# Performance work log

Hardware: AMD Instinct MI355X
Metric: run time of the kernel (lower is better)

The kernel has to match this reference:

```python
import jax, jax.numpy as jnp
import numpy as np

H_DIM = 32
EPS = 1e-7


def setup_inputs() -> dict:
    key = jax.random.key(0)
    ks = jax.random.split(key, 9)
    B, L, I = 2048, 256, 8
    return {
        "X": jax.random.normal(ks[0], (B, L, I), dtype=jnp.float32),
        "y": jax.random.randint(ks[1], (B,), 0, 2, dtype=jnp.int64),
        "W1": jax.random.normal(ks[2], (I, H_DIM), dtype=jnp.float32),
        "cls_tok": jax.random.normal(ks[3], (H_DIM,), dtype=jnp.float32),
        "W_q": jax.random.normal(ks[4], (H_DIM, H_DIM), dtype=jnp.float32),
        "W_k": jax.random.normal(ks[5], (H_DIM, H_DIM), dtype=jnp.float32),
        "W_v": jax.random.normal(ks[6], (H_DIM, H_DIM), dtype=jnp.float32),
        "W_t": jax.random.normal(ks[7], (H_DIM, H_DIM), dtype=jnp.float32),
        "W2": jax.random.normal(ks[8], (H_DIM, 2), dtype=jnp.float32),
    }


def reference(X, y, W1, cls_tok, W_q, W_k, W_v, W_t, W2):
    B = X.shape[0]
    # global mean/std normalization (torch.std is unbiased, ddof=1)
    h_pre1 = (X - X.mean()) / (X.std(ddof=1) + EPS)
    h_1 = h_pre1 @ W1                                   # [B, L, H]
    cls = jnp.broadcast_to(cls_tok[None, None, :], (B, 1, H_DIM))
    h_pre2 = jnp.concatenate([h_1, cls], axis=1)        # [B, L+1, H]
    Q = h_pre2 @ W_q
    K = h_pre2 @ W_k
    V = h_pre2 @ W_v
    S = jax.nn.softmax(jnp.einsum('bqh,bkh->bqk', Q, K) / jnp.sqrt(jnp.float32(H_DIM)), axis=-1)
    h_2 = jnp.einsum('bqk,bkh->bqh', S, V) + h_pre2 @ W_t
    z = h_2[:, -1] @ W2                                 # [B, o_dim]
    log_s = jax.nn.log_softmax(z, axis=-1)
    loss = -jnp.take_along_axis(log_s, y[:, None], axis=1)[:, 0].mean()
    return loss
```

## Files before the change

kernel.cpp:

```cpp
#include <hip/hip_runtime.h>

#define N_TOTAL 4194304
#define B_SIZE  2048
#define L_SIZE  256
#define I_DIM   8
#define H       32
#define K1_BLK  256

#define CRAW_OFF 4096
#define ACC_OFF  4112
#define FIXSCALE 4294967296.0
#define MASK56   0x00FFFFFFFFFFFFFFull

__global__ __launch_bounds__(1024) void k1_stats(
    const float4* __restrict__ X4,
    const float* __restrict__ W1, const float* __restrict__ cls,
    const float* __restrict__ Wq, const float* __restrict__ Wk,
    const float* __restrict__ Wv, const float* __restrict__ Wt,
    const float* __restrict__ W2, double* __restrict__ dws)
{
    const int t = threadIdx.x, b = blockIdx.x;
    const int lane = t & 63, wid = t >> 6;
    const int g = b * 1024 + t;

    float s1 = 0.f, s2 = 0.f;
    #pragma unroll
    for (int i = 0; i < 4; i++) {
        float4 v = X4[g + i * 262144];
        s1 += v.x + v.y + v.z + v.w;
        s2 += v.x * v.x + v.y * v.y + v.z * v.z + v.w * v.w;
    }
    for (int off = 32; off; off >>= 1) {
        s1 += __shfl_down(s1, off);
        s2 += __shfl_down(s2, off);
    }
    __shared__ float a1[16], a2[16];
    if (lane == 0) { a1[wid] = s1; a2[wid] = s2; }
    __syncthreads();
    if (t == 0) {
        float r1 = 0.f, r2 = 0.f;
        #pragma unroll
        for (int i = 0; i < 16; i++) { r1 += a1[i]; r2 += a2[i]; }
        dws[16 * b]     = (double)r1;
        dws[16 * b + 1] = (double)r2;
    }

    if (b == 0) {
        __shared__ float qv[H], kcls[H], vcls[H], tv[H], gg[H], WV[I_DIM][H];
        const float rs32 = 0.17677669529663687f;
        float* craw = (float*)(dws + CRAW_OFF);
        if (t < H) {
            const int h = t;
            float q_ = 0.f, k_ = 0.f, v_ = 0.f, t_ = 0.f;
            for (int j = 0; j < H; j++) {
                float cj = cls[j];
                q_ += cj * Wq[j * H + h];
                k_ += cj * Wk[j * H + h];
                v_ += cj * Wv[j * H + h];
                t_ += cj * Wt[j * H + h];
            }
            qv[h] = q_; kcls[h] = k_; vcls[h] = v_; tv[h] = t_;
        }
        __syncthreads();
        if (t < H) {
            const int h = t;
            float g_ = 0.f;
            for (int j = 0; j < H; j++) g_ += Wk[h * H + j] * qv[j];
            gg[h] = g_;
            for (int i = 0; i < I_DIM; i++) {
                float a = 0.f;
                for (int j = 0; j < H; j++) a += W1[i * H + j] * Wv[j * H + h];
                WV[i][h] = a;
            }
        }
        __syncthreads();
        if (t < I_DIM) {
            float a = 0.f;
            for (int j = 0; j < H; j++) a += W1[t * H + j] * gg[j];
            craw[t] = a;
        }
        if (t < I_DIM * 2) {
            const int i = t >> 1, o = t & 1;
            float a = 0.f;
            for (int j = 0; j < H; j++) a += WV[i][j] * W2[j * 2 + o];
            craw[10 + i * 2 + o] = a;
        }
        if (t == 0) {
            float c2 = 0.f;
            for (int j = 0; j < H; j++) c2 += qv[j] * kcls[j];
            craw[9] = c2 * rs32;
            float vw0 = 0.f, vw1 = 0.f, tw0 = 0.f, tw1 = 0.f;
            for (int j = 0; j < H; j++) {
                vw0 += vcls[j] * W2[j * 2];     vw1 += vcls[j] * W2[j * 2 + 1];
                tw0 += tv[j]   * W2[j * 2];     tw1 += tv[j]   * W2[j * 2 + 1];
            }
            craw[28] = vw0; craw[29] = vw1; craw[30] = tw0; craw[31] = tw1;
            *(unsigned long long*)(dws + ACC_OFF) = 0ull;
        }
    }
}

__global__ __launch_bounds__(512) void k2_attn(
    const float* __restrict__ X, const int* __restrict__ y,
    double* __restrict__ dws, float* __restrict__ out)
{
    const int t = threadIdx.x, b = blockIdx.x;
    const int lane = t & 63, w = t >> 6;

    __shared__ double da[4], db[4];
    __shared__ float cst[32];
    __shared__ double wloss[8];

    if (t < 256) {
        double d1 = dws[16 * t], d2 = dws[16 * t + 1];
        for (int off = 32; off; off >>= 1) {
            d1 += __shfl_down(d1, off);
            d2 += __shfl_down(d2, off);
        }
        if (lane == 0) { da[w] = d1; db[w] = d2; }
    }
    __syncthreads();
    const double S1 = da[0] + da[1] + da[2] + da[3];
    const double S2 = db[0] + db[1] + db[2] + db[3];
    const double mu = S1 / (double)N_TOTAL;
    const double var = (S2 - S1 * S1 / (double)N_TOTAL) / (double)(N_TOTAL - 1);
    const float sdev = (float)(sqrt(var) + 1e-7);
    const float negmu = (float)(-mu);

    const float* craw = (const float*)(dws + CRAW_OFF);
    const float rs32 = 0.17677669529663687f;
    if (t < 32) {
        if (t < 8) {
            cst[t] = craw[t] / sdev * rs32;
        } else if (t == 8) {
            float cs = 0.f;
            for (int i = 0; i < 8; i++) cs += craw[i] / sdev * rs32;
            cst[8] = negmu * cs;
        } else if (t == 9) {
            cst[9] = craw[9];
        } else if (t < 26) {
            cst[t] = craw[t] / sdev;
        } else if (t == 26) {
            float m0 = 0.f;
            for (int i = 0; i < 8; i++) m0 += craw[10 + 2 * i] / sdev;
            cst[26] = negmu * m0;
        } else if (t == 27) {
            float m1 = 0.f;
            for (int i = 0; i < 8; i++) m1 += craw[11 + 2 * i] / sdev;
            cst[27] = negmu * m1;
        } else {
            cst[t] = craw[t];
        }
    }
    __syncthreads();

    const int r = b * 8 + w;
    const float4* Xb = (const float4*)(X + (size_t)r * (L_SIZE * I_DIM));
    float x[4][8];
    float sc[4];
    const float c8 = cst[8];
    float u0 = cst[0], u1 = cst[1], u2 = cst[2], u3 = cst[3];
    float u4 = cst[4], u5 = cst[5], u6 = cst[6], u7 = cst[7];
    #pragma unroll
    for (int j = 0; j < 4; j++) {
        const int p = 64 * j + lane;
        float4 p0 = Xb[2 * p], p1 = Xb[2 * p + 1];
        x[j][0] = p0.x; x[j][1] = p0.y; x[j][2] = p0.z; x[j][3] = p0.w;
        x[j][4] = p1.x; x[j][5] = p1.y; x[j][6] = p1.z; x[j][7] = p1.w;
        sc[j] = c8 + x[j][0] * u0 + x[j][1] * u1 + x[j][2] * u2 + x[j][3] * u3
                   + x[j][4] * u4 + x[j][5] * u5 + x[j][6] * u6 + x[j][7] * u7;
    }

    float m = fmaxf(fmaxf(sc[0], sc[1]), fmaxf(sc[2], sc[3]));
    for (int off = 32; off; off >>= 1) m = fmaxf(m, __shfl_xor(m, off));
    m = fmaxf(m, cst[9]);

    float v[9];
    #pragma unroll
    for (int j2 = 0; j2 < 9; j2++) v[j2] = 0.f;
    #pragma unroll
    for (int j = 0; j < 4; j++) {
        float e = expf(sc[j] - m);
        v[0] += e;
        #pragma unroll
        for (int i = 0; i < 8; i++) v[i + 1] += e * x[j][i];
    }
    for (int off = 32; off; off >>= 1) {
        #pragma unroll
        for (int j2 = 0; j2 < 9; j2++) v[j2] += __shfl_down(v[j2], off);
    }

    if (lane == 0) {
        float se = v[0];
        float ecls = expf(cst[9] - m);
        float inv = 1.f / (se + ecls);
        float S256 = ecls * inv;
        float z[2];
        #pragma unroll
        for (int o = 0; o < 2; o++) {
            float a = 0.f;
            #pragma unroll
            for (int i = 0; i < 8; i++)
                a += (v[i + 1] * inv) * cst[10 + i * 2 + o];
            z[o] = a + (1.f - S256) * cst[26 + o] + S256 * cst[28 + o] + cst[30 + o];
        }
        float zm = fmaxf(z[0], z[1]);
        float lse = zm + logf(expf(z[0] - zm) + expf(z[1] - zm));
        int yb = y[r];
        wloss[w] = (double)(lse - z[yb]);
    }
    __syncthreads();

    if (t == 0) {
        double blockloss = 0.0;
        #pragma unroll
        for (int i = 0; i < 8; i++) blockloss += wloss[i];
        unsigned long long fixed =
            (unsigned long long)(blockloss * FIXSCALE + 0.5);
        unsigned long long* acc = (unsigned long long*)(dws + ACC_OFF);
        unsigned long long old = __hip_atomic_fetch_add(
            acc, fixed + (1ull << 56), __ATOMIC_RELAXED, __HIP_MEMORY_SCOPE_AGENT);
        if ((old >> 56) == 255ull) {
            unsigned long long total = ((old & MASK56) + fixed) & MASK56;
            out[0] = (float)((double)total / FIXSCALE / (double)B_SIZE);
        }
    }
}

extern "C" void kernel_launch(void* const* d_in, const int* in_sizes, int n_in,
                              void* d_out, int out_size, void* d_ws, size_t ws_size,
                              hipStream_t stream) {
    const float* X   = (const float*)d_in[0];
    const int*   y   = (const int*)d_in[1];
    const float* W1  = (const float*)d_in[2];
    const float* cls = (const float*)d_in[3];
    const float* Wq  = (const float*)d_in[4];
    const float* Wk  = (const float*)d_in[5];
    const float* Wv  = (const float*)d_in[6];
    const float* Wt  = (const float*)d_in[7];
    const float* W2  = (const float*)d_in[8];
    float* out = (float*)d_out;
    double* dws = (double*)d_ws;

    hipLaunchKernelGGL(k1_stats, dim3(K1_BLK), dim3(1024), 0, stream,
                       (const float4*)X, W1, cls, Wq, Wk, Wv, Wt, W2, dws);
    hipLaunchKernelGGL(k2_attn, dim3(K1_BLK), dim3(512), 0, stream,
                       X, y, dws, out);
}
```

Baseline: 21.72 us.

## Split each row across two waves and issue X loads before stats reduction

The attention kernel now uses 1024 threads per block, with two wavefronts per batch row instead of one, and combines their partial max and sums through shared memory. X loads are issued at kernel start, before the global-stats reduction and constant setup, so memory latency overlaps with that prologue. The per-block stats in the workspace are packed densely instead of being strided by 16 doubles. The cost is extra barriers and a cross-wave combine step done by 8 threads.

Result: slower. 23.02 us (+6.0%).

```diff
diff --git a/kernel.cpp b/kernel.cpp
--- a/kernel.cpp
+++ b/kernel.cpp
@@ -6,9 +6,10 @@
 #define I_DIM   8
 #define H       32
 #define K1_BLK  256
-
-#define CRAW_OFF 4096
-#define ACC_OFF  4112
+#define K2_BLK  256
+
+#define CRAW_OFF 1024
+#define ACC_OFF  1040
 #define FIXSCALE 4294967296.0
 #define MASK56   0x00FFFFFFFFFFFFFFull
 
@@ -41,8 +42,8 @@
         float r1 = 0.f, r2 = 0.f;
         #pragma unroll
         for (int i = 0; i < 16; i++) { r1 += a1[i]; r2 += a2[i]; }
-        dws[16 * b]     = (double)r1;
-        dws[16 * b + 1] = (double)r2;
+        dws[2 * b]     = (double)r1;
+        dws[2 * b + 1] = (double)r2;
     }
 
     if (b == 0) {
@@ -100,19 +101,23 @@
     }
 }
 
-__global__ __launch_bounds__(512) void k2_attn(
+__global__ __launch_bounds__(1024) void k2_attn(
     const float* __restrict__ X, const int* __restrict__ y,
     double* __restrict__ dws, float* __restrict__ out)
 {
     const int t = threadIdx.x, b = blockIdx.x;
     const int lane = t & 63, w = t >> 6;
+    const int lr = w >> 1, half = w & 1;
+    const int r = b * 8 + lr;
+
+    const float4* Xb = (const float4*)X + (size_t)r * 512;
+    const int p0 = half * 128 + lane;
+    float4 A = Xb[2 * p0],        Bv = Xb[2 * p0 + 1];
+    float4 C = Xb[2 * (p0 + 64)], D  = Xb[2 * (p0 + 64) + 1];
 
     __shared__ double da[4], db[4];
-    __shared__ float cst[32];
-    __shared__ double wloss[8];
-
     if (t < 256) {
-        double d1 = dws[16 * t], d2 = dws[16 * t + 1];
+        double d1 = dws[2 * t], d2 = dws[2 * t + 1];
         for (int off = 32; off; off >>= 1) {
             d1 += __shfl_down(d1, off);
             d2 += __shfl_down(d2, off);
@@ -120,16 +125,23 @@
         if (lane == 0) { da[w] = d1; db[w] = d2; }
     }
     __syncthreads();
-    const double S1 = da[0] + da[1] + da[2] + da[3];
-    const double S2 = db[0] + db[1] + db[2] + db[3];
-    const double mu = S1 / (double)N_TOTAL;
-    const double var = (S2 - S1 * S1 / (double)N_TOTAL) / (double)(N_TOTAL - 1);
-    const float sdev = (float)(sqrt(var) + 1e-7);
-    const float negmu = (float)(-mu);
-
+
+    __shared__ float sNegMu, sSdev;
+    if (t == 0) {
+        double S1 = da[0] + da[1] + da[2] + da[3];
+        double S2 = db[0] + db[1] + db[2] + db[3];
+        double mu = S1 / (double)N_TOTAL;
+        double var = (S2 - S1 * S1 / (double)N_TOTAL) / (double)(N_TOTAL - 1);
+        sSdev = (float)(sqrt(var) + 1e-7);
+        sNegMu = (float)(-mu);
+    }
+    __syncthreads();
+
+    __shared__ float cst[32];
     const float* craw = (const float*)(dws + CRAW_OFF);
     const float rs32 = 0.17677669529663687f;
     if (t < 32) {
+        const float sdev = sSdev, negmu = sNegMu;
         if (t < 8) {
             cst[t] = craw[t] / sdev * rs32;
         } else if (t == 8) {
@@ -154,46 +166,47 @@
     }
     __syncthreads();
 
-    const int r = b * 8 + w;
-    const float4* Xb = (const float4*)(X + (size_t)r * (L_SIZE * I_DIM));
-    float x[4][8];
-    float sc[4];
+    float x0[8] = {A.x, A.y, A.z, A.w, Bv.x, Bv.y, Bv.z, Bv.w};
+    float x1[8] = {C.x, C.y, C.z, C.w, D.x,  D.y,  D.z,  D.w};
     const float c8 = cst[8];
-    float u0 = cst[0], u1 = cst[1], u2 = cst[2], u3 = cst[3];
-    float u4 = cst[4], u5 = cst[5], u6 = cst[6], u7 = cst[7];
+    float sc0 = c8, sc1 = c8;
     #pragma unroll
-    for (int j = 0; j < 4; j++) {
-        const int p = 64 * j + lane;
-        float4 p0 = Xb[2 * p], p1 = Xb[2 * p + 1];
-        x[j][0] = p0.x; x[j][1] = p0.y; x[j][2] = p0.z; x[j][3] = p0.w;
-        x[j][4] = p1.x; x[j][5] = p1.y; x[j][6] = p1.z; x[j][7] = p1.w;
-        sc[j] = c8 + x[j][0] * u0 + x[j][1] * u1 + x[j][2] * u2 + x[j][3] * u3
-                   + x[j][4] * u4 + x[j][5] * u5 + x[j][6] * u6 + x[j][7] * u7;
-    }
-
-    float m = fmaxf(fmaxf(sc[0], sc[1]), fmaxf(sc[2], sc[3]));
-    for (int off = 32; off; off >>= 1) m = fmaxf(m, __shfl_xor(m, off));
-    m = fmaxf(m, cst[9]);
-
+    for (int i = 0; i < 8; i++) {
+        sc0 += x0[i] * cst[i];
+        sc1 += x1[i] * cst[i];
+    }
+
+    __shared__ float rmax[8][2];
+    __shared__ float rsum[8][2][9];
+    __shared__ double wloss[8];
+    float mw = fmaxf(sc0, sc1);
+    for (int off = 32; off; off >>= 1) mw = fmaxf(mw, __shfl_xor(mw, off));
+    if (lane == 0) rmax[lr][half] = mw;
+    __syncthreads();
+    const float m = fmaxf(fmaxf(rmax[lr][0], rmax[lr][1]), cst[9]);
+
+    float e0 = expf(sc0 - m), e1 = expf(sc1 - m);
     float v[9];
+    v[0] = e0 + e1;
     #pragma unroll
-    for (int j2 = 0; j2 < 9; j2++) v[j2] = 0.f;
-    #pragma unroll
-    for (int j = 0; j < 4; j++) {
-        float e = expf(sc[j] - m);
-        v[0] += e;
-        #pragma unroll
-        for (int i = 0; i < 8; i++) v[i + 1] += e * x[j][i];
-    }
+    for (int i = 0; i < 8; i++) v[i + 1] = e0 * x0[i] + e1 * x1[i];
     for (int off = 32; off; off >>= 1) {
         #pragma unroll
-        for (int j2 = 0; j2 < 9; j2++) v[j2] += __shfl_down(v[j2], off);
-    }
-
+        for (int j = 0; j < 9; j++) v[j] += __shfl_down(v[j], off);
+    }
     if (lane == 0) {
-        float se = v[0];
-        float ecls = expf(cst[9] - m);
-        float inv = 1.f / (se + ecls);
+        #pragma unroll
+        for (int j = 0; j < 9; j++) rsum[lr][half][j] = v[j];
+    }
+    __syncthreads();
+
+    if (t < 8) {
+        float vv[9];
+        #pragma unroll
+        for (int j = 0; j < 9; j++) vv[j] = rsum[t][0][j] + rsum[t][1][j];
+        float mrow = fmaxf(fmaxf(rmax[t][0], rmax[t][1]), cst[9]);
+        float ecls = expf(cst[9] - mrow);
+        float inv = 1.f / (vv[0] + ecls);
         float S256 = ecls * inv;
         float z[2];
         #pragma unroll
@@ -201,13 +214,13 @@
             float a = 0.f;
             #pragma unroll
             for (int i = 0; i < 8; i++)
-                a += (v[i + 1] * inv) * cst[10 + i * 2 + o];
+                a += (vv[i + 1] * inv) * cst[10 + i * 2 + o];
             z[o] = a + (1.f - S256) * cst[26 + o] + S256 * cst[28 + o] + cst[30 + o];
         }
         float zm = fmaxf(z[0], z[1]);
         float lse = zm + logf(expf(z[0] - zm) + expf(z[1] - zm));
-        int yb = y[r];
-        wloss[w] = (double)(lse - z[yb]);
+        int yb = y[b * 8 + t];
+        wloss[t] = (double)(lse - z[yb]);
     }
     __syncthreads();
 
@@ -220,7 +233,7 @@
         unsigned long long* acc = (unsigned long long*)(dws + ACC_OFF);
         unsigned long long old = __hip_atomic_fetch_add(
             acc, fixed + (1ull << 56), __ATOMIC_RELAXED, __HIP_MEMORY_SCOPE_AGENT);
-        if ((old >> 56) == 255ull) {
+        if ((old >> 56) == (unsigned long long)(K2_BLK - 1)) {
             unsigned long long total = ((old & MASK56) + fixed) & MASK56;
             out[0] = (float)((double)total / FIXSCALE / (double)B_SIZE);
         }
@@ -244,6 +257,6 @@
 
     hipLaunchKernelGGL(k1_stats, dim3(K1_BLK), dim3(1024), 0, stream,
                        (const float4*)X, W1, cls, Wq, Wk, Wv, Wt, W2, dws);
-    hipLaunchKernelGGL(k2_attn, dim3(K1_BLK), dim3(512), 0, stream,
+    hipLaunchKernelGGL(k2_attn, dim3(K2_BLK), dim3(1024), 0, stream,
                        X, y, dws, out);
 }
```
